# Performance work log

Measured on AMD Instinct MI355X. Metric: run time of the kernel, lower is better.

## Reference

```python
import jax, jax.numpy as jnp
import numpy as np

DIM = 1024
NUM_HEADS = 16
HEAD_DIM = DIM // NUM_HEADS
ROPE_BASE = 10000.0


def _rope_cos_sin(seq_len, head_dim):
    inv_freq = 1.0 / (ROPE_BASE ** (jnp.arange(0, head_dim, 2, dtype=jnp.float32) / head_dim))
    t = jnp.arange(seq_len, dtype=jnp.float32)
    freqs = t[:, None] * inv_freq[None, :]            # [S, Dh/2]
    emb = jnp.concatenate([freqs, freqs], axis=-1)    # [S, Dh]
    return jnp.cos(emb), jnp.sin(emb)


def _rotate_half(x):
    half = x.shape[-1] // 2
    return jnp.concatenate([-x[..., half:], x[..., :half]], axis=-1)


def setup_inputs() -> dict:
    key = jax.random.key(0)
    k1, k2, k3 = jax.random.split(key, 3)
    B, S = 2, 2048
    x = jax.random.normal(k1, (B, S, DIM), dtype=jnp.float32)
    w_qkv = jax.random.normal(k2, (3 * DIM, DIM), dtype=jnp.float32) * (DIM ** -0.5)
    w_out = jax.random.normal(k3, (DIM, DIM), dtype=jnp.float32) * (DIM ** -0.5)
    return {"x": x, "w_qkv": w_qkv, "w_out": w_out}


def reference(x, w_qkv, w_out):
    B, S, D = x.shape
    H, Dh = NUM_HEADS, HEAD_DIM
    scale = Dh ** -0.5

    qkv = (x @ w_qkv.T).reshape(B, S, 3, H, Dh)      # [B,S,3,H,Dh]
    qkv = jnp.transpose(qkv, (2, 0, 3, 1, 4))        # [3,B,H,S,Dh]
    q, k, v = qkv[0], qkv[1], qkv[2]

    cos, sin = _rope_cos_sin(S, Dh)                  # [S,Dh]
    cos = cos[None, None, :, :]
    sin = sin[None, None, :, :]
    q = q * cos + _rotate_half(q) * sin
    k = k * cos + _rotate_half(k) * sin

    scores = jnp.einsum('bhqd,bhkd->bhqk', q, k) * scale
    causal_mask = jnp.triu(jnp.ones((S, S), dtype=bool), k=1)
    scores = jnp.where(causal_mask[None, None], -jnp.inf, scores)
    attn = jax.nn.softmax(scores, axis=-1)
    out = jnp.einsum('bhqk,bhkd->bhqd', attn, v)      # [B,H,S,Dh]
    out = jnp.transpose(out, (0, 2, 1, 3)).reshape(B, S, D)
    return out @ w_out.T
```

## Files before the change

kernel.cpp:

```cpp
#include <hip/hip_runtime.h>
#include <stdint.h>

typedef uint16_t u16;
typedef __attribute__((ext_vector_type(8))) short bf16x8;
typedef __attribute__((ext_vector_type(4))) float f32x4;

__device__ inline u16 f2b(float f) {
  uint32_t u = __float_as_uint(f);
  u += 0x7FFF + ((u >> 16) & 1);
  return (u16)(u >> 16);
}
__device__ inline float b2f(u16 h) {
  return __uint_as_float(((uint32_t)h) << 16);
}

typedef __attribute__((address_space(1))) void gvoid;
typedef __attribute__((address_space(3))) void lvoid;
#define GLOAD16(gp, lp)                                                        \
  __builtin_amdgcn_global_load_lds((gvoid*)(gp), (lvoid*)(lp), 16, 0, 0)

__device__ __forceinline__ int probe_mode(const u16* __restrict__ P, int t,
                                          int* cnt_sh) {
  if (t == 0) *cnt_sh = 0;
  __syncthreads();
  float av = fabsf(b2f(P[t * 2]));
  if (av >= 1000.0f) atomicAdd(cnt_sh, 1);
  __syncthreads();
  return (*cnt_sh > 16) ? 1 : 0;
}

__global__ __launch_bounds__(256) void k_qkv_rope(const void* __restrict__ Xv,
                                                  const void* __restrict__ Wv,
                                                  u16* __restrict__ Qo,
                                                  u16* __restrict__ Ko,
                                                  u16* __restrict__ Vo) {
  __shared__ u16 As[2][2][64][40];
  __shared__ u16 Bs[2][3][64][40];
  __shared__ float Cs[64][66];
  __shared__ int cnt_sh;
  const int t = threadIdx.x, w = t >> 6, lane = t & 63;
  const int mode = probe_mode((const u16*)Xv, t, &cnt_sh);
  const int id = blockIdx.y * 16 + blockIdx.x;
  const int xcd = id & 7, p = id >> 3;
  const int h = p >> 2;
  const int n0h = h * 64;
  const int m0 = ((xcd << 2) | (p & 3)) << 7;
  const int lr = lane & 15, lq = lane >> 4;
  f32x4 acc[3][2][4] = {};
  const int rA = t >> 2, cA = (t & 3) * 8;
  const int aoff0 = (m0 + rA) * 1024 + cA;
  const int aoff1 = (m0 + 64 + rA) * 1024 + cA;
  const int boff0 = (n0h + rA) * 1024 + cA;

  if (mode == 0) {
    const u16* Xp = (const u16*)Xv;
    const u16* Wp = (const u16*)Wv;
    uint4 pa0 = *(const uint4*)(Xp + aoff0);
    uint4 pa1 = *(const uint4*)(Xp + aoff1);
    uint4 pb0 = *(const uint4*)(Wp + boff0);
    uint4 pb1 = *(const uint4*)(Wp + boff0 + 1048576);
    uint4 pb2 = *(const uint4*)(Wp + boff0 + 2097152);
    *(uint4*)&As[0][0][rA][cA] = pa0;
    *(uint4*)&As[0][1][rA][cA] = pa1;
    *(uint4*)&Bs[0][0][rA][cA] = pb0;
    *(uint4*)&Bs[0][1][rA][cA] = pb1;
    *(uint4*)&Bs[0][2][rA][cA] = pb2;
    pa0 = *(const uint4*)(Xp + aoff0 + 32);
    pa1 = *(const uint4*)(Xp + aoff1 + 32);
    pb0 = *(const uint4*)(Wp + boff0 + 32);
    pb1 = *(const uint4*)(Wp + boff0 + 1048576 + 32);
    pb2 = *(const uint4*)(Wp + boff0 + 2097152 + 32);
    __syncthreads();
    int cur = 0;
    for (int k0 = 0; k0 < 1024; k0 += 32) {
      if (k0 + 32 < 1024) {
        *(uint4*)&As[cur ^ 1][0][rA][cA] = pa0;
        *(uint4*)&As[cur ^ 1][1][rA][cA] = pa1;
        *(uint4*)&Bs[cur ^ 1][0][rA][cA] = pb0;
        *(uint4*)&Bs[cur ^ 1][1][rA][cA] = pb1;
        *(uint4*)&Bs[cur ^ 1][2][rA][cA] = pb2;
      }
      if (k0 + 64 < 1024) {
        const int kn = k0 + 64;
        pa0 = *(const uint4*)(Xp + aoff0 + kn);
        pa1 = *(const uint4*)(Xp + aoff1 + kn);
        pb0 = *(const uint4*)(Wp + boff0 + kn);
        pb1 = *(const uint4*)(Wp + boff0 + 1048576 + kn);
        pb2 = *(const uint4*)(Wp + boff0 + 2097152 + kn);
      }
      bf16x8 bf[3];
#pragma unroll
      for (int e = 0; e < 3; ++e)
        bf[e] = *(const bf16x8*)&Bs[cur][e][(w << 4) + lr][lq * 8];
#pragma unroll
      for (int mt = 0; mt < 4; ++mt) {
        bf16x8 af0 = *(const bf16x8*)&As[cur][0][(mt << 4) + lr][lq * 8];
        bf16x8 af1 = *(const bf16x8*)&As[cur][1][(mt << 4) + lr][lq * 8];
#pragma unroll
        for (int e = 0; e < 3; ++e) {
          acc[e][0][mt] = __builtin_amdgcn_mfma_f32_16x16x32_bf16(af0, bf[e], acc[e][0][mt], 0, 0, 0);
          acc[e][1][mt] = __builtin_amdgcn_mfma_f32_16x16x32_bf16(af1, bf[e], acc[e][1][mt], 0, 0, 0);
        }
      }
      __syncthreads();
      cur ^= 1;
    }
  } else {
    for (int k0 = 0; k0 < 1024; k0 += 32) {
      __syncthreads();
      const float* Xf = (const float*)Xv;
      const float* Wf = (const float*)Wv;
#pragma unroll
      for (int ee = 0; ee < 8; ++ee) {
        As[0][0][rA][cA + ee] = f2b(Xf[aoff0 + k0 + ee]);
        As[0][1][rA][cA + ee] = f2b(Xf[aoff1 + k0 + ee]);
        Bs[0][0][rA][cA + ee] = f2b(Wf[boff0 + k0 + ee]);
        Bs[0][1][rA][cA + ee] = f2b(Wf[boff0 + 1048576 + k0 + ee]);
        Bs[0][2][rA][cA + ee] = f2b(Wf[boff0 + 2097152 + k0 + ee]);
      }
      __syncthreads();
      bf16x8 bf[3];
#pragma unroll
      for (int e = 0; e < 3; ++e)
        bf[e] = *(const bf16x8*)&Bs[0][e][(w << 4) + lr][lq * 8];
#pragma unroll
      for (int mt = 0; mt < 4; ++mt) {
        bf16x8 af0 = *(const bf16x8*)&As[0][0][(mt << 4) + lr][lq * 8];
        bf16x8 af1 = *(const bf16x8*)&As[0][1][(mt << 4) + lr][lq * 8];
#pragma unroll
        for (int e = 0; e < 3; ++e) {
          acc[e][0][mt] = __builtin_amdgcn_mfma_f32_16x16x32_bf16(af0, bf[e], acc[e][0][mt], 0, 0, 0);
          acc[e][1][mt] = __builtin_amdgcn_mfma_f32_16x16x32_bf16(af1, bf[e], acc[e][1][mt], 0, 0, 0);
        }
      }
    }
  }

  for (int f = 0; f < 2; ++f) {
    const int m0f = m0 + f * 64;
    for (int e = 0; e < 3; ++e) {
      __syncthreads();
      {
        const int col = (w << 4) + lr;
#pragma unroll
        for (int mt = 0; mt < 4; ++mt)
#pragma unroll
          for (int i = 0; i < 4; ++i)
            Cs[mt * 16 + lq * 4 + i][col] = acc[e][f][mt][i];
      }
      __syncthreads();
      if (e == 2) {
        const int sx = t & 63, dh0 = (t >> 6) * 16;
        const int m = m0f + sx, b = m >> 11, s = m & 2047;
        const long hb = (long)(b * 16 + h) * 64;
#pragma unroll
        for (int u = 0; u < 16; ++u) {
          int dh = dh0 + u;
          Vo[(hb + dh) * 2048 + s] = f2b(Cs[sx][dh]);
        }
      } else {
        const int r = t >> 2, dh0 = (t & 3) * 16;
        const int m = m0f + r, b = m >> 11, s = m & 2047;
        const int obase = ((b * 16 + h) * 2048 + s) * 64;
        u16* O = (e == 0) ? Qo : Ko;
#pragma unroll
        for (int u = 0; u < 16; ++u) {
          int dh = dh0 + u;
          float v  = Cs[r][dh];
          float vp = Cs[r][dh ^ 32];
          float sign = (dh < 32) ? -1.0f : 1.0f;
          float fr  = __expf((float)(dh & 31) * -0.28782314f);
          float ang = (float)s * fr;
          float sn = __sinf(ang), cs = __cosf(ang);
          O[obase + dh] = f2b(v * cs + sign * vp * sn);
        }
      }
    }
  }
}

__device__ __forceinline__ void attn_tile(u16 QP[64][72], u16 Ks[64][72],
                                          u16 Vt[64][72], const bf16x8 qf[2],
                                          f32x4 o_acc[4], float& m_i, float& l_i,
                                          int kt, int qt_tile, int w, int lr,
                                          int lq, int lq4, int base16, int qrow_l) {
  f32x4 sa[4] = {};
#pragma unroll
  for (int mb = 0; mb < 4; ++mb)
#pragma unroll
    for (int kk = 0; kk < 2; ++kk) {
      bf16x8 kf = *(const bf16x8*)&Ks[mb * 16 + lr][kk * 32 + lq * 8];
      sa[mb] = __builtin_amdgcn_mfma_f32_16x16x32_bf16(kf, qf[kk], sa[mb], 0, 0, 0);
    }
  float sc[4][4];
  float m_new = m_i;
#pragma unroll
  for (int mb = 0; mb < 4; ++mb)
#pragma unroll
    for (int i = 0; i < 4; ++i) {
      float sv = sa[mb][i] * 0.125f;
      if (kt == qt_tile && (mb * 16 + lq4 + i) > qrow_l) sv = -3.0e4f;
      sc[mb][i] = sv;
      m_new = fmaxf(m_new, sv);
    }
  m_new = fmaxf(m_new, __shfl_xor(m_new, 16));
  m_new = fmaxf(m_new, __shfl_xor(m_new, 32));
  float alpha = __expf(m_i - m_new);
  m_i = m_new;
  float p[4][4], sm = 0.f;
#pragma unroll
  for (int mb = 0; mb < 4; ++mb)
#pragma unroll
    for (int i = 0; i < 4; ++i) { p[mb][i] = __expf(sc[mb][i] - m_new); sm += p[mb][i]; }
  sm += __shfl_xor(sm, 16);
  sm += __shfl_xor(sm, 32);
  l_i = l_i * alpha + sm;
#pragma unroll
  for (int mb = 0; mb < 4; ++mb) {
    uint2 pk;
    pk.x = (uint32_t)f2b(p[mb][0]) | ((uint32_t)f2b(p[mb][1]) << 16);
    pk.y = (uint32_t)f2b(p[mb][2]) | ((uint32_t)f2b(p[mb][3]) << 16);
    *(uint2*)&QP[w * 16 + lr][mb * 16 + lq4] = pk;
  }
#pragma unroll
  for (int i = 0; i < 4; ++i) {
    float ai = __shfl(alpha, base16 | (lq4 + i));
    o_acc[0][i] *= ai; o_acc[1][i] *= ai;
    o_acc[2][i] *= ai; o_acc[3][i] *= ai;
  }
  asm volatile("s_waitcnt lgkmcnt(0)" ::: "memory");
#pragma unroll
  for (int kk = 0; kk < 2; ++kk) {
    bf16x8 pf = *(const bf16x8*)&QP[w * 16 + lr][kk * 32 + lq * 8];
#pragma unroll
    for (int nb = 0; nb < 4; ++nb) {
      bf16x8 vf = *(const bf16x8*)&Vt[nb * 16 + lr][kk * 32 + lq * 8];
      o_acc[nb] = __builtin_amdgcn_mfma_f32_16x16x32_bf16(pf, vf, o_acc[nb], 0, 0, 0);
    }
  }
}

__global__ __launch_bounds__(256) void k_attn(const u16* __restrict__ Q,
                                              const u16* __restrict__ K,
                                              const u16* __restrict__ V,
                                              u16* __restrict__ AO) {
  __shared__ u16 QP[64][72];
  __shared__ u16 Ks[2][64][72];
  __shared__ u16 Vt[2][64][72];
  const int id = blockIdx.y * 16 + blockIdx.x;
  const int xcd = id & 7, p = id >> 3;
  const int bh = (xcd << 2) | (p & 3);
  const int qp = p >> 2;
  const int qtA = 31 - qp;
  const int qtB = qp;
  const int b = bh >> 4, h = bh & 15;
  const u16* Qg = Q + (bh * 2048) * 64;
  const u16* Kg = K + bh * 2048 * 64;
  const u16* Vg = V + (long)bh * 64 * 2048;
  const int t = threadIdx.x, w = t >> 6, lane = t & 63;
  const int lr = lane & 15, lq = lane >> 4;
  const int lq4 = lq * 4;
  const int base16 = lane & 48;
  const int r0 = t >> 3, c0 = (t & 7) * 8;
  const int qrow_l = w * 16 + lr;

  uint4 pk0 = *(const uint4*)&Kg[r0 * 64 + c0];
  uint4 pk1 = *(const uint4*)&Kg[(r0 + 32) * 64 + c0];
  uint4 pv0 = *(const uint4*)&Vg[r0 * 2048 + c0];
  uint4 pv1 = *(const uint4*)&Vg[(r0 + 32) * 2048 + c0];

  bf16x8 qfA[2], qfB[2];
  *(uint4*)&QP[r0][c0]      = *(const uint4*)&Qg[(qtA * 64 + r0) * 64 + c0];
  *(uint4*)&QP[r0 + 32][c0] = *(const uint4*)&Qg[(qtA * 64 + r0 + 32) * 64 + c0];
  __syncthreads();
#pragma unroll
  for (int kk = 0; kk < 2; ++kk)
    qfA[kk] = *(const bf16x8*)&QP[w * 16 + lr][kk * 32 + lq * 8];
  __syncthreads();
  *(uint4*)&QP[r0][c0]      = *(const uint4*)&Qg[(qtB * 64 + r0) * 64 + c0];
  *(uint4*)&QP[r0 + 32][c0] = *(const uint4*)&Qg[(qtB * 64 + r0 + 32) * 64 + c0];
  __syncthreads();
#pragma unroll
  for (int kk = 0; kk < 2; ++kk)
    qfB[kk] = *(const bf16x8*)&QP[w * 16 + lr][kk * 32 + lq * 8];

  *(uint4*)&Ks[0][r0][c0]      = pk0;
  *(uint4*)&Ks[0][r0 + 32][c0] = pk1;
  *(uint4*)&Vt[0][r0][c0]      = pv0;
  *(uint4*)&Vt[0][r0 + 32][c0] = pv1;
  pk0 = *(const uint4*)&Kg[(64 + r0) * 64 + c0];
  pk1 = *(const uint4*)&Kg[(64 + r0 + 32) * 64 + c0];
  pv0 = *(const uint4*)&Vg[r0 * 2048 + 64 + c0];
  pv1 = *(const uint4*)&Vg[(r0 + 32) * 2048 + 64 + c0];
  __syncthreads();

  float m_iA = -3.0e4f, l_iA = 0.f, m_iB = -3.0e4f, l_iB = 0.f;
  f32x4 o_accA[4] = {}, o_accB[4] = {};

  int cur = 0;
  for (int kt = 0; kt <= qtA; ++kt) {
    if (kt + 1 <= qtA) {
      *(uint4*)&Ks[cur ^ 1][r0][c0]      = pk0;
      *(uint4*)&Ks[cur ^ 1][r0 + 32][c0] = pk1;
      *(uint4*)&Vt[cur ^ 1][r0][c0]      = pv0;
      *(uint4*)&Vt[cur ^ 1][r0 + 32][c0] = pv1;
    }
    if (kt + 2 <= qtA) {
      const int kn = kt + 2;
      pk0 = *(const uint4*)&Kg[(kn * 64 + r0) * 64 + c0];
      pk1 = *(const uint4*)&Kg[(kn * 64 + r0 + 32) * 64 + c0];
      pv0 = *(const uint4*)&Vg[r0 * 2048 + kn * 64 + c0];
      pv1 = *(const uint4*)&Vg[(r0 + 32) * 2048 + kn * 64 + c0];
    }

    attn_tile(QP, Ks[cur], Vt[cur], qfA, o_accA, m_iA, l_iA, kt, qtA,
              w, lr, lq, lq4, base16, qrow_l);
    if (kt <= qtB) {
      asm volatile("s_waitcnt lgkmcnt(0)" ::: "memory");
      attn_tile(QP, Ks[cur], Vt[cur], qfB, o_accB, m_iB, l_iB, kt, qtB,
                w, lr, lq, lq4, base16, qrow_l);
    }
    __syncthreads();
    cur ^= 1;
  }
  float linvA = 1.0f / l_iA, linvB = 1.0f / l_iB;
#pragma unroll
  for (int i = 0; i < 4; ++i) {
    float invA = __shfl(linvA, base16 | (lq4 + i));
    float invB = __shfl(linvB, base16 | (lq4 + i));
    int rowA = qtA * 64 + w * 16 + lq4 + i;
    int rowB = qtB * 64 + w * 16 + lq4 + i;
    int obA = (b * 2048 + rowA) * 1024 + h * 64;
    int obB = (b * 2048 + rowB) * 1024 + h * 64;
#pragma unroll
    for (int nb = 0; nb < 4; ++nb) {
      AO[obA + nb * 16 + lr] = f2b(o_accA[nb][i] * invA);
      AO[obB + nb * 16 + lr] = f2b(o_accB[nb][i] * invB);
    }
  }
}

__global__ __launch_bounds__(256) void k_gemm_out(const u16* __restrict__ A,
                                                  const void* __restrict__ Bv,
                                                  void* __restrict__ Cv) {
  __shared__ u16 As[2][64][64];
  __shared__ u16 Bs[2][2][64][64];
  __shared__ int cnt_sh;
  const int t = threadIdx.x, w = t >> 6, lane = t & 63;
  const int mode = probe_mode((const u16*)Bv, t, &cnt_sh);
  const int id = blockIdx.y * 8 + blockIdx.x;
  const int xcd = id & 7, p = id >> 3;
  const int n0 = (p >> 3) * 128;
  const int m0 = ((xcd << 3) | (p & 7)) * 64;
  const int lr = lane & 15, lq = lane >> 4;
  f32x4 acc[2][4] = {};

  if (mode == 0) {
    const u16* Bp = (const u16*)Bv;
    const int lrow = lane >> 3;
    const int lg   = (lane & 7) ^ lrow;
    const long ar0 = (long)(m0 + w * 8 + lrow) * 1024 + lg * 8;
    const long ar1 = (long)(m0 + w * 8 + 32 + lrow) * 1024 + lg * 8;
    const long br00 = (long)(n0 + w * 8 + lrow) * 1024 + lg * 8;
    const long br01 = (long)(n0 + w * 8 + 32 + lrow) * 1024 + lg * 8;
    const long br10 = br00 + 65536;
    const long br11 = br01 + 65536;
#define STAGE_OUT(buf, kk)                                                     \
    do {                                                                       \
      GLOAD16(A + ar0 + (kk),   &As[buf][w * 8][0]);                           \
      GLOAD16(A + ar1 + (kk),   &As[buf][w * 8 + 32][0]);                      \
      GLOAD16(Bp + br00 + (kk), &Bs[buf][0][w * 8][0]);                        \
      GLOAD16(Bp + br01 + (kk), &Bs[buf][0][w * 8 + 32][0]);                   \
      GLOAD16(Bp + br10 + (kk), &Bs[buf][1][w * 8][0]);                        \
      GLOAD16(Bp + br11 + (kk), &Bs[buf][1][w * 8 + 32][0]);                   \
    } while (0)
    STAGE_OUT(0, 0);
    asm volatile("s_waitcnt vmcnt(0)" ::: "memory");
    __syncthreads();
    int cur = 0;
    for (int k0 = 0; k0 < 1024; k0 += 64) {
      if (k0 + 64 < 1024) STAGE_OUT(cur ^ 1, k0 + 64);
#pragma unroll
      for (int kk = 0; kk < 2; ++kk) {
        bf16x8 bfx[2];
        const int rowB = (w << 4) + lr;
        const int gB = ((kk * 4 + lq) ^ (rowB & 7)) * 8;
#pragma unroll
        for (int e = 0; e < 2; ++e)
          bfx[e] = *(const bf16x8*)&Bs[cur][e][rowB][gB];
#pragma unroll
        for (int mt = 0; mt < 4; ++mt) {
          const int rowA = (mt << 4) + lr;
          const int gA = ((kk * 4 + lq) ^ (rowA & 7)) * 8;
          bf16x8 af = *(const bf16x8*)&As[cur][rowA][gA];
#pragma unroll
          for (int e = 0; e < 2; ++e)
            acc[e][mt] = __builtin_amdgcn_mfma_f32_16x16x32_bf16(af, bfx[e], acc[e][mt], 0, 0, 0);
        }
      }
      __syncthreads();
      cur ^= 1;
    }
#undef STAGE_OUT
  } else {
    const float* Bf = (const float*)Bv;
    const int r = t >> 2, cc = (t & 3) * 16;
    for (int k0 = 0; k0 < 1024; k0 += 64) {
      __syncthreads();
      *(uint4*)&As[0][r][cc]     = *(const uint4*)(A + (long)(m0 + r) * 1024 + k0 + cc);
      *(uint4*)&As[0][r][cc + 8] = *(const uint4*)(A + (long)(m0 + r) * 1024 + k0 + cc + 8);
#pragma unroll
      for (int ee = 0; ee < 16; ++ee) {
        Bs[0][0][r][cc + ee] = f2b(Bf[(long)(n0 + r) * 1024 + k0 + cc + ee]);
        Bs[0][1][r][cc + ee] = f2b(Bf[(long)(n0 + 64 + r) * 1024 + k0 + cc + ee]);
      }
      __syncthreads();
#pragma unroll
      for (int kk = 0; kk < 2; ++kk) {
        bf16x8 bfx[2];
        const int rowB = (w << 4) + lr;
#pragma unroll
        for (int e = 0; e < 2; ++e)
          bfx[e] = *(const bf16x8*)&Bs[0][e][rowB][kk * 32 + lq * 8];
#pragma unroll
        for (int mt = 0; mt < 4; ++mt) {
          bf16x8 af = *(const bf16x8*)&As[0][(mt << 4) + lr][kk * 32 + lq * 8];
#pragma unroll
          for (int e = 0; e < 2; ++e)
            acc[e][mt] = __builtin_amdgcn_mfma_f32_16x16x32_bf16(af, bfx[e], acc[e][mt], 0, 0, 0);
        }
      }
    }
  }
#pragma unroll
  for (int e = 0; e < 2; ++e) {
    const int col = n0 + e * 64 + (w << 4) + lr;
    if (mode == 0) {
      u16* C = (u16*)Cv;
#pragma unroll
      for (int mt = 0; mt < 4; ++mt)
#pragma unroll
        for (int i = 0; i < 4; ++i)
          C[(m0 + mt * 16 + lq * 4 + i) * 1024 + col] = f2b(acc[e][mt][i]);
    } else {
      float* C = (float*)Cv;
#pragma unroll
      for (int mt = 0; mt < 4; ++mt)
#pragma unroll
        for (int i = 0; i < 4; ++i)
          C[(m0 + mt * 16 + lq * 4 + i) * 1024 + col] = acc[e][mt][i];
    }
  }
}

extern "C" void kernel_launch(void* const* d_in, const int* in_sizes, int n_in,
                              void* d_out, int out_size, void* d_ws, size_t ws_size,
                              hipStream_t stream) {
  const void* x    = d_in[0];
  const void* wqkv = d_in[1];
  const void* wout = d_in[2];

  u16* qb = (u16*)((char*)d_ws + 256);
  u16* kb = qb + 4194304;
  u16* vb = kb + 4194304;
  u16* ao = vb + 4194304;

  k_qkv_rope<<<dim3(16, 32), 256, 0, stream>>>(x, wqkv, qb, kb, vb);
  k_attn    <<<dim3(16, 32), 256, 0, stream>>>(qb, kb, vb, ao);
  k_gemm_out<<<dim3(8, 64), 256, 0, stream>>>(ao, wout, d_out);
}
```

Measured before the change: 201.9 us.

## Read K and V fragments directly from global memory instead of LDS staging

The attention kernel no longer stages K and V tiles through double-buffered shared memory with register prefetch and a per-iteration barrier. Each wave now loads its MFMA fragments for K and V straight from global memory, and a separate P buffer is used for the second query tile. This removes the LDS writes and __syncthreads, but each wave re-reads K/V from global/L2 without any software prefetch, so load latency may be exposed.

```diff
diff --git a/kernel.cpp b/kernel.cpp
--- a/kernel.cpp
+++ b/kernel.cpp
@@ -179,19 +179,10 @@
   }
 }
 
-__device__ __forceinline__ void attn_tile(u16 QP[64][72], u16 Ks[64][72],
-                                          u16 Vt[64][72], const bf16x8 qf[2],
-                                          f32x4 o_acc[4], float& m_i, float& l_i,
-                                          int kt, int qt_tile, int w, int lr,
-                                          int lq, int lq4, int base16, int qrow_l) {
-  f32x4 sa[4] = {};
-#pragma unroll
-  for (int mb = 0; mb < 4; ++mb)
-#pragma unroll
-    for (int kk = 0; kk < 2; ++kk) {
-      bf16x8 kf = *(const bf16x8*)&Ks[mb * 16 + lr][kk * 32 + lq * 8];
-      sa[mb] = __builtin_amdgcn_mfma_f32_16x16x32_bf16(kf, qf[kk], sa[mb], 0, 0, 0);
-    }
+__device__ __forceinline__ void softmax_tile(const f32x4 sa[4], u16 P[64][72],
+                                             f32x4 o_acc[4], float& m_i, float& l_i,
+                                             int kt, int qt_tile, int w, int lr,
+                                             int lq4, int base16, int qrow_l) {
   float sc[4][4];
   float m_new = m_i;
 #pragma unroll
@@ -207,36 +198,26 @@
   m_new = fmaxf(m_new, __shfl_xor(m_new, 32));
   float alpha = __expf(m_i - m_new);
   m_i = m_new;
-  float p[4][4], sm = 0.f;
+  float pv[4][4], sm = 0.f;
 #pragma unroll
   for (int mb = 0; mb < 4; ++mb)
 #pragma unroll
-    for (int i = 0; i < 4; ++i) { p[mb][i] = __expf(sc[mb][i] - m_new); sm += p[mb][i]; }
+    for (int i = 0; i < 4; ++i) { pv[mb][i] = __expf(sc[mb][i] - m_new); sm += pv[mb][i]; }
   sm += __shfl_xor(sm, 16);
   sm += __shfl_xor(sm, 32);
   l_i = l_i * alpha + sm;
 #pragma unroll
   for (int mb = 0; mb < 4; ++mb) {
     uint2 pk;
-    pk.x = (uint32_t)f2b(p[mb][0]) | ((uint32_t)f2b(p[mb][1]) << 16);
-    pk.y = (uint32_t)f2b(p[mb][2]) | ((uint32_t)f2b(p[mb][3]) << 16);
-    *(uint2*)&QP[w * 16 + lr][mb * 16 + lq4] = pk;
+    pk.x = (uint32_t)f2b(pv[mb][0]) | ((uint32_t)f2b(pv[mb][1]) << 16);
+    pk.y = (uint32_t)f2b(pv[mb][2]) | ((uint32_t)f2b(pv[mb][3]) << 16);
+    *(uint2*)&P[w * 16 + lr][mb * 16 + lq4] = pk;
   }
 #pragma unroll
   for (int i = 0; i < 4; ++i) {
     float ai = __shfl(alpha, base16 | (lq4 + i));
     o_acc[0][i] *= ai; o_acc[1][i] *= ai;
     o_acc[2][i] *= ai; o_acc[3][i] *= ai;
-  }
-  asm volatile("s_waitcnt lgkmcnt(0)" ::: "memory");
-#pragma unroll
-  for (int kk = 0; kk < 2; ++kk) {
-    bf16x8 pf = *(const bf16x8*)&QP[w * 16 + lr][kk * 32 + lq * 8];
-#pragma unroll
-    for (int nb = 0; nb < 4; ++nb) {
-      bf16x8 vf = *(const bf16x8*)&Vt[nb * 16 + lr][kk * 32 + lq * 8];
-      o_acc[nb] = __builtin_amdgcn_mfma_f32_16x16x32_bf16(pf, vf, o_acc[nb], 0, 0, 0);
-    }
   }
 }
 
@@ -245,8 +226,7 @@
                                               const u16* __restrict__ V,
                                               u16* __restrict__ AO) {
   __shared__ u16 QP[64][72];
-  __shared__ u16 Ks[2][64][72];
-  __shared__ u16 Vt[2][64][72];
+  __shared__ u16 PB[64][72];
   const int id = blockIdx.y * 16 + blockIdx.x;
   const int xcd = id & 7, p = id >> 3;
   const int bh = (xcd << 2) | (p & 3);
@@ -264,11 +244,6 @@
   const int r0 = t >> 3, c0 = (t & 7) * 8;
   const int qrow_l = w * 16 + lr;
 
-  uint4 pk0 = *(const uint4*)&Kg[r0 * 64 + c0];
-  uint4 pk1 = *(const uint4*)&Kg[(r0 + 32) * 64 + c0];
-  uint4 pv0 = *(const uint4*)&Vg[r0 * 2048 + c0];
-  uint4 pv1 = *(const uint4*)&Vg[(r0 + 32) * 2048 + c0];
-
   bf16x8 qfA[2], qfB[2];
   *(uint4*)&QP[r0][c0]      = *(const uint4*)&Qg[(qtA * 64 + r0) * 64 + c0];
   *(uint4*)&QP[r0 + 32][c0] = *(const uint4*)&Qg[(qtA * 64 + r0 + 32) * 64 + c0];
@@ -283,45 +258,57 @@
 #pragma unroll
   for (int kk = 0; kk < 2; ++kk)
     qfB[kk] = *(const bf16x8*)&QP[w * 16 + lr][kk * 32 + lq * 8];
-
-  *(uint4*)&Ks[0][r0][c0]      = pk0;
-  *(uint4*)&Ks[0][r0 + 32][c0] = pk1;
-  *(uint4*)&Vt[0][r0][c0]      = pv0;
-  *(uint4*)&Vt[0][r0 + 32][c0] = pv1;
-  pk0 = *(const uint4*)&Kg[(64 + r0) * 64 + c0];
-  pk1 = *(const uint4*)&Kg[(64 + r0 + 32) * 64 + c0];
-  pv0 = *(const uint4*)&Vg[r0 * 2048 + 64 + c0];
-  pv1 = *(const uint4*)&Vg[(r0 + 32) * 2048 + 64 + c0];
   __syncthreads();
 
   float m_iA = -3.0e4f, l_iA = 0.f, m_iB = -3.0e4f, l_iB = 0.f;
   f32x4 o_accA[4] = {}, o_accB[4] = {};
 
-  int cur = 0;
   for (int kt = 0; kt <= qtA; ++kt) {
-    if (kt + 1 <= qtA) {
-      *(uint4*)&Ks[cur ^ 1][r0][c0]      = pk0;
-      *(uint4*)&Ks[cur ^ 1][r0 + 32][c0] = pk1;
-      *(uint4*)&Vt[cur ^ 1][r0][c0]      = pv0;
-      *(uint4*)&Vt[cur ^ 1][r0 + 32][c0] = pv1;
-    }
-    if (kt + 2 <= qtA) {
-      const int kn = kt + 2;
-      pk0 = *(const uint4*)&Kg[(kn * 64 + r0) * 64 + c0];
-      pk1 = *(const uint4*)&Kg[(kn * 64 + r0 + 32) * 64 + c0];
-      pv0 = *(const uint4*)&Vg[r0 * 2048 + kn * 64 + c0];
-      pv1 = *(const uint4*)&Vg[(r0 + 32) * 2048 + kn * 64 + c0];
-    }
-
-    attn_tile(QP, Ks[cur], Vt[cur], qfA, o_accA, m_iA, l_iA, kt, qtA,
-              w, lr, lq, lq4, base16, qrow_l);
+    const u16* Kt = Kg + kt * 4096;
+    const int vc = kt * 64;
+    f32x4 sa[4];
+#pragma unroll
+    for (int mb = 0; mb < 4; ++mb) {
+      sa[mb] = (f32x4){0.f, 0.f, 0.f, 0.f};
+#pragma unroll
+      for (int kk = 0; kk < 2; ++kk) {
+        bf16x8 kf = *(const bf16x8*)&Kt[(mb * 16 + lr) * 64 + kk * 32 + lq * 8];
+        sa[mb] = __builtin_amdgcn_mfma_f32_16x16x32_bf16(kf, qfA[kk], sa[mb], 0, 0, 0);
+      }
+    }
+    softmax_tile(sa, QP, o_accA, m_iA, l_iA, kt, qtA, w, lr, lq4, base16, qrow_l);
+    asm volatile("s_waitcnt lgkmcnt(0)" ::: "memory");
+#pragma unroll
+    for (int kk = 0; kk < 2; ++kk) {
+      bf16x8 pf = *(const bf16x8*)&QP[w * 16 + lr][kk * 32 + lq * 8];
+#pragma unroll
+      for (int nb = 0; nb < 4; ++nb) {
+        bf16x8 vf = *(const bf16x8*)&Vg[(nb * 16 + lr) * 2048 + vc + kk * 32 + lq * 8];
+        o_accA[nb] = __builtin_amdgcn_mfma_f32_16x16x32_bf16(pf, vf, o_accA[nb], 0, 0, 0);
+      }
+    }
     if (kt <= qtB) {
+#pragma unroll
+      for (int mb = 0; mb < 4; ++mb) {
+        sa[mb] = (f32x4){0.f, 0.f, 0.f, 0.f};
+#pragma unroll
+        for (int kk = 0; kk < 2; ++kk) {
+          bf16x8 kf = *(const bf16x8*)&Kt[(mb * 16 + lr) * 64 + kk * 32 + lq * 8];
+          sa[mb] = __builtin_amdgcn_mfma_f32_16x16x32_bf16(kf, qfB[kk], sa[mb], 0, 0, 0);
+        }
+      }
+      softmax_tile(sa, PB, o_accB, m_iB, l_iB, kt, qtB, w, lr, lq4, base16, qrow_l);
       asm volatile("s_waitcnt lgkmcnt(0)" ::: "memory");
-      attn_tile(QP, Ks[cur], Vt[cur], qfB, o_accB, m_iB, l_iB, kt, qtB,
-                w, lr, lq, lq4, base16, qrow_l);
-    }
-    __syncthreads();
-    cur ^= 1;
+#pragma unroll
+      for (int kk = 0; kk < 2; ++kk) {
+        bf16x8 pf = *(const bf16x8*)&PB[w * 16 + lr][kk * 32 + lq * 8];
+#pragma unroll
+        for (int nb = 0; nb < 4; ++nb) {
+          bf16x8 vf = *(const bf16x8*)&Vg[(nb * 16 + lr) * 2048 + vc + kk * 32 + lq * 8];
+          o_accB[nb] = __builtin_amdgcn_mfma_f32_16x16x32_bf16(pf, vf, o_accB[nb], 0, 0, 0);
+        }
+      }
+    }
   }
   float linvA = 1.0f / l_iA, linvB = 1.0f / l_iB;
 #pragma unroll
```

Result: slower. 270.4 us (+33.9%).

## Use direct global-to-LDS loads with XOR swizzle and K=64 tiles in QKV GEMM

Applied to the files above, without the earlier changes.

The QKV projection GEMM now stages X and W tiles with global_load_lds (asynchronous direct-to-LDS copies) instead of loading through registers. The K step grows from 32 to 64, and an XOR swizzle on the column group avoids LDS bank conflicts now that rows are unpadded. The tile buffers share a union with the epilogue Cs buffer to keep LDS use bounded. The goal is to cut register staging traffic and halve the number of barrier iterations. The cost is larger LDS tiles, which may lower occupancy.

```diff
diff --git a/kernel.cpp b/kernel.cpp
--- a/kernel.cpp
+++ b/kernel.cpp
@@ -34,9 +34,11 @@
                                                   u16* __restrict__ Qo,
                                                   u16* __restrict__ Ko,
                                                   u16* __restrict__ Vo) {
-  __shared__ u16 As[2][2][64][40];
-  __shared__ u16 Bs[2][3][64][40];
-  __shared__ float Cs[64][66];
+  union ShQ {
+    struct { u16 A[2][2][64][64]; u16 B[2][3][64][64]; } st;
+    float Cs[64][66];
+  };
+  __shared__ ShQ sh;
   __shared__ int cnt_sh;
   const int t = threadIdx.x, w = t >> 6, lane = t & 63;
   const int mode = probe_mode((const u16*)Xv, t, &cnt_sh);
@@ -47,90 +49,93 @@
   const int m0 = ((xcd << 2) | (p & 3)) << 7;
   const int lr = lane & 15, lq = lane >> 4;
   f32x4 acc[3][2][4] = {};
-  const int rA = t >> 2, cA = (t & 3) * 8;
-  const int aoff0 = (m0 + rA) * 1024 + cA;
-  const int aoff1 = (m0 + 64 + rA) * 1024 + cA;
-  const int boff0 = (n0h + rA) * 1024 + cA;
 
   if (mode == 0) {
     const u16* Xp = (const u16*)Xv;
     const u16* Wp = (const u16*)Wv;
-    uint4 pa0 = *(const uint4*)(Xp + aoff0);
-    uint4 pa1 = *(const uint4*)(Xp + aoff1);
-    uint4 pb0 = *(const uint4*)(Wp + boff0);
-    uint4 pb1 = *(const uint4*)(Wp + boff0 + 1048576);
-    uint4 pb2 = *(const uint4*)(Wp + boff0 + 2097152);
-    *(uint4*)&As[0][0][rA][cA] = pa0;
-    *(uint4*)&As[0][1][rA][cA] = pa1;
-    *(uint4*)&Bs[0][0][rA][cA] = pb0;
-    *(uint4*)&Bs[0][1][rA][cA] = pb1;
-    *(uint4*)&Bs[0][2][rA][cA] = pb2;
-    pa0 = *(const uint4*)(Xp + aoff0 + 32);
-    pa1 = *(const uint4*)(Xp + aoff1 + 32);
-    pb0 = *(const uint4*)(Wp + boff0 + 32);
-    pb1 = *(const uint4*)(Wp + boff0 + 1048576 + 32);
-    pb2 = *(const uint4*)(Wp + boff0 + 2097152 + 32);
+    const int lrow = lane >> 3;
+    const int lg   = (lane & 7) ^ lrow;
+    const long a0r0 = (long)(m0 + w * 8 + lrow) * 1024 + lg * 8;
+    const long a0r1 = (long)(m0 + w * 8 + 32 + lrow) * 1024 + lg * 8;
+    const long a1r0 = (long)(m0 + 64 + w * 8 + lrow) * 1024 + lg * 8;
+    const long a1r1 = (long)(m0 + 64 + w * 8 + 32 + lrow) * 1024 + lg * 8;
+    const long b_r0 = (long)(n0h + w * 8 + lrow) * 1024 + lg * 8;
+    const long b_r1 = (long)(n0h + w * 8 + 32 + lrow) * 1024 + lg * 8;
+#define STAGE_QKV(buf, kk)                                                     \
+    do {                                                                       \
+      GLOAD16(Xp + a0r0 + (kk),           &sh.st.A[buf][0][w * 8][0]);         \
+      GLOAD16(Xp + a0r1 + (kk),           &sh.st.A[buf][0][w * 8 + 32][0]);    \
+      GLOAD16(Xp + a1r0 + (kk),           &sh.st.A[buf][1][w * 8][0]);         \
+      GLOAD16(Xp + a1r1 + (kk),           &sh.st.A[buf][1][w * 8 + 32][0]);    \
+      GLOAD16(Wp + b_r0 + (kk),           &sh.st.B[buf][0][w * 8][0]);         \
+      GLOAD16(Wp + b_r1 + (kk),           &sh.st.B[buf][0][w * 8 + 32][0]);    \
+      GLOAD16(Wp + b_r0 + 1048576 + (kk), &sh.st.B[buf][1][w * 8][0]);         \
+      GLOAD16(Wp + b_r1 + 1048576 + (kk), &sh.st.B[buf][1][w * 8 + 32][0]);    \
+      GLOAD16(Wp + b_r0 + 2097152 + (kk), &sh.st.B[buf][2][w * 8][0]);         \
+      GLOAD16(Wp + b_r1 + 2097152 + (kk), &sh.st.B[buf][2][w * 8 + 32][0]);    \
+    } while (0)
+    STAGE_QKV(0, 0);
+    asm volatile("s_waitcnt vmcnt(0)" ::: "memory");
     __syncthreads();
     int cur = 0;
-    for (int k0 = 0; k0 < 1024; k0 += 32) {
-      if (k0 + 32 < 1024) {
-        *(uint4*)&As[cur ^ 1][0][rA][cA] = pa0;
-        *(uint4*)&As[cur ^ 1][1][rA][cA] = pa1;
-        *(uint4*)&Bs[cur ^ 1][0][rA][cA] = pb0;
-        *(uint4*)&Bs[cur ^ 1][1][rA][cA] = pb1;
-        *(uint4*)&Bs[cur ^ 1][2][rA][cA] = pb2;
-      }
-      if (k0 + 64 < 1024) {
-        const int kn = k0 + 64;
-        pa0 = *(const uint4*)(Xp + aoff0 + kn);
-        pa1 = *(const uint4*)(Xp + aoff1 + kn);
-        pb0 = *(const uint4*)(Wp + boff0 + kn);
-        pb1 = *(const uint4*)(Wp + boff0 + 1048576 + kn);
-        pb2 = *(const uint4*)(Wp + boff0 + 2097152 + kn);
-      }
-      bf16x8 bf[3];
-#pragma unroll
-      for (int e = 0; e < 3; ++e)
-        bf[e] = *(const bf16x8*)&Bs[cur][e][(w << 4) + lr][lq * 8];
-#pragma unroll
-      for (int mt = 0; mt < 4; ++mt) {
-        bf16x8 af0 = *(const bf16x8*)&As[cur][0][(mt << 4) + lr][lq * 8];
-        bf16x8 af1 = *(const bf16x8*)&As[cur][1][(mt << 4) + lr][lq * 8];
-#pragma unroll
-        for (int e = 0; e < 3; ++e) {
-          acc[e][0][mt] = __builtin_amdgcn_mfma_f32_16x16x32_bf16(af0, bf[e], acc[e][0][mt], 0, 0, 0);
-          acc[e][1][mt] = __builtin_amdgcn_mfma_f32_16x16x32_bf16(af1, bf[e], acc[e][1][mt], 0, 0, 0);
+    for (int k0 = 0; k0 < 1024; k0 += 64) {
+      if (k0 + 64 < 1024) STAGE_QKV(cur ^ 1, k0 + 64);
+#pragma unroll
+      for (int kk = 0; kk < 2; ++kk) {
+        bf16x8 bf[3];
+        const int rowB = (w << 4) + lr;
+        const int gB = ((kk * 4 + lq) ^ (rowB & 7)) * 8;
+#pragma unroll
+        for (int e = 0; e < 3; ++e)
+          bf[e] = *(const bf16x8*)&sh.st.B[cur][e][rowB][gB];
+#pragma unroll
+        for (int mt = 0; mt < 4; ++mt) {
+          const int rowA = (mt << 4) + lr;
+          const int gA = ((kk * 4 + lq) ^ (rowA & 7)) * 8;
+          bf16x8 af0 = *(const bf16x8*)&sh.st.A[cur][0][rowA][gA];
+          bf16x8 af1 = *(const bf16x8*)&sh.st.A[cur][1][rowA][gA];
+#pragma unroll
+          for (int e = 0; e < 3; ++e) {
+            acc[e][0][mt] = __builtin_amdgcn_mfma_f32_16x16x32_bf16(af0, bf[e], acc[e][0][mt], 0, 0, 0);
+            acc[e][1][mt] = __builtin_amdgcn_mfma_f32_16x16x32_bf16(af1, bf[e], acc[e][1][mt], 0, 0, 0);
+          }
         }
       }
       __syncthreads();
       cur ^= 1;
     }
+#undef STAGE_QKV
   } else {
-    for (int k0 = 0; k0 < 1024; k0 += 32) {
-      __syncthreads();
-      const float* Xf = (const float*)Xv;
-      const float* Wf = (const float*)Wv;
-#pragma unroll
-      for (int ee = 0; ee < 8; ++ee) {
-        As[0][0][rA][cA + ee] = f2b(Xf[aoff0 + k0 + ee]);
-        As[0][1][rA][cA + ee] = f2b(Xf[aoff1 + k0 + ee]);
-        Bs[0][0][rA][cA + ee] = f2b(Wf[boff0 + k0 + ee]);
-        Bs[0][1][rA][cA + ee] = f2b(Wf[boff0 + 1048576 + k0 + ee]);
-        Bs[0][2][rA][cA + ee] = f2b(Wf[boff0 + 2097152 + k0 + ee]);
-      }
-      __syncthreads();
-      bf16x8 bf[3];
-#pragma unroll
-      for (int e = 0; e < 3; ++e)
-        bf[e] = *(const bf16x8*)&Bs[0][e][(w << 4) + lr][lq * 8];
-#pragma unroll
-      for (int mt = 0; mt < 4; ++mt) {
-        bf16x8 af0 = *(const bf16x8*)&As[0][0][(mt << 4) + lr][lq * 8];
-        bf16x8 af1 = *(const bf16x8*)&As[0][1][(mt << 4) + lr][lq * 8];
-#pragma unroll
-        for (int e = 0; e < 3; ++e) {
-          acc[e][0][mt] = __builtin_amdgcn_mfma_f32_16x16x32_bf16(af0, bf[e], acc[e][0][mt], 0, 0, 0);
-          acc[e][1][mt] = __builtin_amdgcn_mfma_f32_16x16x32_bf16(af1, bf[e], acc[e][1][mt], 0, 0, 0);
+    const float* Xf = (const float*)Xv;
+    const float* Wf = (const float*)Wv;
+    const int r = t >> 2, cc = (t & 3) * 16;
+    for (int k0 = 0; k0 < 1024; k0 += 64) {
+      __syncthreads();
+#pragma unroll
+      for (int ee = 0; ee < 16; ++ee) {
+        sh.st.A[0][0][r][cc + ee] = f2b(Xf[(long)(m0 + r) * 1024 + k0 + cc + ee]);
+        sh.st.A[0][1][r][cc + ee] = f2b(Xf[(long)(m0 + 64 + r) * 1024 + k0 + cc + ee]);
+        sh.st.B[0][0][r][cc + ee] = f2b(Wf[(long)(n0h + r) * 1024 + k0 + cc + ee]);
+        sh.st.B[0][1][r][cc + ee] = f2b(Wf[(long)(n0h + r) * 1024 + 1048576 + k0 + cc + ee]);
+        sh.st.B[0][2][r][cc + ee] = f2b(Wf[(long)(n0h + r) * 1024 + 2097152 + k0 + cc + ee]);
+      }
+      __syncthreads();
+#pragma unroll
+      for (int kk = 0; kk < 2; ++kk) {
+        bf16x8 bf[3];
+        const int rowB = (w << 4) + lr;
+#pragma unroll
+        for (int e = 0; e < 3; ++e)
+          bf[e] = *(const bf16x8*)&sh.st.B[0][e][rowB][kk * 32 + lq * 8];
+#pragma unroll
+        for (int mt = 0; mt < 4; ++mt) {
+          bf16x8 af0 = *(const bf16x8*)&sh.st.A[0][0][(mt << 4) + lr][kk * 32 + lq * 8];
+          bf16x8 af1 = *(const bf16x8*)&sh.st.A[0][1][(mt << 4) + lr][kk * 32 + lq * 8];
+#pragma unroll
+          for (int e = 0; e < 3; ++e) {
+            acc[e][0][mt] = __builtin_amdgcn_mfma_f32_16x16x32_bf16(af0, bf[e], acc[e][0][mt], 0, 0, 0);
+            acc[e][1][mt] = __builtin_amdgcn_mfma_f32_16x16x32_bf16(af1, bf[e], acc[e][1][mt], 0, 0, 0);
+          }
         }
       }
     }
@@ -146,7 +151,7 @@
         for (int mt = 0; mt < 4; ++mt)
 #pragma unroll
           for (int i = 0; i < 4; ++i)
-            Cs[mt * 16 + lq * 4 + i][col] = acc[e][f][mt][i];
+            sh.Cs[mt * 16 + lq * 4 + i][col] = acc[e][f][mt][i];
       }
       __syncthreads();
       if (e == 2) {
@@ -156,7 +161,7 @@
 #pragma unroll
         for (int u = 0; u < 16; ++u) {
           int dh = dh0 + u;
-          Vo[(hb + dh) * 2048 + s] = f2b(Cs[sx][dh]);
+          Vo[(hb + dh) * 2048 + s] = f2b(sh.Cs[sx][dh]);
         }
       } else {
         const int r = t >> 2, dh0 = (t & 3) * 16;
@@ -166,8 +171,8 @@
 #pragma unroll
         for (int u = 0; u < 16; ++u) {
           int dh = dh0 + u;
-          float v  = Cs[r][dh];
-          float vp = Cs[r][dh ^ 32];
+          float v  = sh.Cs[r][dh];
+          float vp = sh.Cs[r][dh ^ 32];
           float sign = (dh < 32) ? -1.0f : 1.0f;
           float fr  = __expf((float)(dh & 31) * -0.28782314f);
           float ang = (float)s * fr;
```

Result: slower. 410.0 us (+103.0%).
